# Performance work log

Hardware: AMD Instinct MI355X
Metric: run time of the kernel (lower is better)

The kernel has to match this reference:

```python
import jax, jax.numpy as jnp
import numpy as np

# torch.linspace(512, 16, 3).int() -> [512, 264, 16]
RES = (512, 264, 16)
FEAT = 4
EMBED_DIM = 1 + FEAT * len(RES)  # 13
HID = 64
N = 4194304


def _linear_init(key, fan_in, fan_out):
    k1, k2 = jax.random.split(key)
    bound = 1.0 / np.sqrt(fan_in)
    w = jax.random.uniform(k1, (fan_in, fan_out), jnp.float32, -bound, bound)
    b = jax.random.uniform(k2, (fan_out,), jnp.float32, -bound, bound)
    return w, b


def setup_inputs() -> dict:
    key = jax.random.key(0)
    ks = jax.random.split(key, 8)
    x = jax.random.uniform(ks[0], (N, 3), jnp.float32)  # [idf, u, v], uv in [0,1)
    tabs = []
    for i, r in enumerate(RES):
        tabs.append(jax.random.uniform(ks[1 + i], ((r + 1) * (r + 1), FEAT),
                                       jnp.float32, -1e-4, 1e-4))
    w1, b1 = _linear_init(ks[4], EMBED_DIM, HID)
    w2, b2 = _linear_init(ks[5], HID, HID)
    w3, b3 = _linear_init(ks[6], HID, 3)
    return {"x": x, "emb0": tabs[0], "emb1": tabs[1], "emb2": tabs[2],
            "w1": w1, "b1": b1, "w2": w2, "b2": b2, "w3": w3, "b3": b3}


def _grid_features(uv, tables):
    feats = []
    for tab, res in zip(tables, RES):
        sx = uv[:, 0] * res
        sy = uv[:, 1] * res
        x0 = sx.astype(jnp.int32)
        y0 = sy.astype(jnp.int32)
        wx = (sx - x0.astype(jnp.float32))[:, None]
        wy = (sy - y0.astype(jnp.float32))[:, None]
        x1 = jnp.minimum(x0 + 1, res)
        y1 = jnp.minimum(y0 + 1, res)
        # note: stride is res (not res+1), faithful to the original code
        v00 = tab[y0 * res + x0]
        v10 = tab[y0 * res + x1]
        v01 = tab[y1 * res + x0]
        v11 = tab[y1 * res + x1]
        top = v00 * (1.0 - wx) + v10 * wx
        bot = v01 * (1.0 - wx) + v11 * wx
        feats.append(top * (1.0 - wy) + bot * wy)
    return jnp.concatenate(feats, axis=1)


def reference(x, emb0, emb1, emb2, w1, b1, w2, b2, w3, b3):
    idf = x[:, :1]
    uv = x[:, 1:3]
    dgf = _grid_features(uv, (emb0, emb1, emb2))
    h = jnp.concatenate([idf, dgf], axis=1)  # [N, 13]
    h = jax.nn.relu(h @ w1 + b1)
    h = jax.nn.relu(h @ w2 + b2)
    return h @ w3 + b3  # [N, 3]
```

## Files before the change

### kernel.cpp

```cpp
#include <hip/hip_runtime.h>

typedef _Float16 half8 __attribute__((ext_vector_type(8)));
typedef _Float16 half4 __attribute__((ext_vector_type(4)));
typedef _Float16 h2    __attribute__((ext_vector_type(2)));
typedef __fp16  fp16x2 __attribute__((ext_vector_type(2)));
typedef float floatx4 __attribute__((ext_vector_type(4)));
typedef float floatx2 __attribute__((ext_vector_type(2)));
typedef int   intx4  __attribute__((ext_vector_type(4)));
typedef intx4 intx4a __attribute__((aligned(8)));

#define TPB 256
#define SCALE   8192.0f
#define INVSC   0.0001220703125f

#define N0E (512 * 512 + 1)
#define N1E (264 * 264 + 1)
#define NC2 (16 * 16)

struct GAddr { int i00, i10, i01, i11; float wx, wy; };

__device__ __forceinline__ GAddr gaddr(int res, float u, float v) {
    float r = (float)res;
    float sx = u * r, sy = v * r;
    int x0 = (int)sx, y0 = (int)sy;
    float wx = sx - (float)x0, wy = sy - (float)y0;
    int x1 = min(x0 + 1, res), y1 = min(y0 + 1, res);
    GAddr g;
    g.i00 = y0 * res + x0;  g.i10 = y0 * res + x1;
    g.i01 = y1 * res + x0;  g.i11 = y1 * res + x1;
    g.wx = wx; g.wy = wy;
    return g;
}

struct GQ { int c; float wx, wy; };

__device__ __forceinline__ GQ gq(int res, float u, float v) {
    float r = (float)res;
    float sx = u * r, sy = v * r;
    int x0 = (int)sx, y0 = (int)sy;
    GQ g; g.c = y0 * res + x0; g.wx = sx - (float)x0; g.wy = sy - (float)y0;
    return g;
}

__device__ __forceinline__ void bil4(float4 v00, float4 v10, float4 v01, float4 v11,
                                     float wx, float wy, float* f) {
    float omx = 1.0f - wx, omy = 1.0f - wy;
    f[0] = (v00.x * omx + v10.x * wx) * omy + (v01.x * omx + v11.x * wx) * wy;
    f[1] = (v00.y * omx + v10.y * wx) * omy + (v01.y * omx + v11.y * wx) * wy;
    f[2] = (v00.z * omx + v10.z * wx) * omy + (v01.z * omx + v11.z * wx) * wy;
    f[3] = (v00.w * omx + v10.w * wx) * omy + (v01.w * omx + v11.w * wx) * wy;
}

__device__ __forceinline__ h2 pk2(float a, float b) {
    fp16x2 r = __builtin_amdgcn_cvt_pkrtz(a, b);
    union { fp16x2 f; h2 h; } u; u.f = r; return u.h;
}

__device__ __forceinline__ void bil8(intx4 q, float wx, float omyS, float wyS, float* f) {
    floatx2 a00 = __builtin_amdgcn_cvt_pk_f32_fp8(q.x, false);
    floatx2 b00 = __builtin_amdgcn_cvt_pk_f32_fp8(q.x, true);
    floatx2 a01 = __builtin_amdgcn_cvt_pk_f32_fp8(q.y, false);
    floatx2 b01 = __builtin_amdgcn_cvt_pk_f32_fp8(q.y, true);
    floatx2 a10 = __builtin_amdgcn_cvt_pk_f32_fp8(q.z, false);
    floatx2 b10 = __builtin_amdgcn_cvt_pk_f32_fp8(q.z, true);
    floatx2 a11 = __builtin_amdgcn_cvt_pk_f32_fp8(q.w, false);
    floatx2 b11 = __builtin_amdgcn_cvt_pk_f32_fp8(q.w, true);
    float omx = 1.0f - wx;
    f[0] = (a00[0] * omx + a10[0] * wx) * omyS + (a01[0] * omx + a11[0] * wx) * wyS;
    f[1] = (a00[1] * omx + a10[1] * wx) * omyS + (a01[1] * omx + a11[1] * wx) * wyS;
    f[2] = (b00[0] * omx + b10[0] * wx) * omyS + (b01[0] * omx + b11[0] * wx) * wyS;
    f[3] = (b00[1] * omx + b10[1] * wx) * omyS + (b01[1] * omx + b11[1] * wx) * wyS;
}

__device__ __forceinline__ void bilq(half8 q0, half8 q1, float wx, float wy, h2* f) {
    h2 wx2  = pk2(wx, wx),           wy2  = pk2(wy, wy);
    h2 omx2 = pk2(1.f - wx, 1.f - wx), omy2 = pk2(1.f - wy, 1.f - wy);
    union { half8 v; h2 p[4]; } a, b;
    a.v = q0; b.v = q1;
    h2 t0 = a.p[0] * omx2 + a.p[2] * wx2;
    h2 t1 = a.p[1] * omx2 + a.p[3] * wx2;
    h2 c0 = b.p[0] * omx2 + b.p[2] * wx2;
    h2 c1 = b.p[1] * omx2 + b.p[3] * wx2;
    f[0] = t0 * omy2 + c0 * wy2;
    f[1] = t1 * omy2 + c1 * wy2;
}

__device__ __forceinline__ half4 relu_pk4(float a, float b, float c, float d) {
    union { half4 v; h2 p[2]; } u;
    u.p[0] = pk2(a, b);
    u.p[1] = pk2(c, d);
    half4 z = {(_Float16)0, (_Float16)0, (_Float16)0, (_Float16)0};
    return __builtin_elementwise_max(u.v, z);
}

__device__ __forceinline__ half4 relu_pk4f(float a, float b, float c, float d) {
    union { half4 v; fp16x2 p[2]; } u;
    u.p[0] = __builtin_amdgcn_cvt_pkrtz(fmaxf(a, 0.0f), fmaxf(b, 0.0f));
    u.p[1] = __builtin_amdgcn_cvt_pkrtz(fmaxf(c, 0.0f), fmaxf(d, 0.0f));
    return u.v;
}

__global__ void pack_tables(const float4* __restrict__ e0,
                            const float4* __restrict__ e1,
                            const float4* __restrict__ e2,
                            int* __restrict__ w)
{
    int i = blockIdx.x * blockDim.x + threadIdx.x;
    if (i < N0E) {
        float4 A = e0[i];
        float4 C = e0[i + 512];
        int d0 = __builtin_amdgcn_cvt_pk_fp8_f32(A.x * SCALE, A.y * SCALE, 0, false);
        d0     = __builtin_amdgcn_cvt_pk_fp8_f32(A.z * SCALE, A.w * SCALE, d0, true);
        int d1 = __builtin_amdgcn_cvt_pk_fp8_f32(C.x * SCALE, C.y * SCALE, 0, false);
        d1     = __builtin_amdgcn_cvt_pk_fp8_f32(C.z * SCALE, C.w * SCALE, d1, true);
        w[2 * i] = d0; w[2 * i + 1] = d1;
    } else if (i < N0E + N1E) {
        int c = i - N0E;
        float4 A = e1[c];
        float4 C = e1[c + 264];
        int d0 = __builtin_amdgcn_cvt_pk_fp8_f32(A.x * SCALE, A.y * SCALE, 0, false);
        d0     = __builtin_amdgcn_cvt_pk_fp8_f32(A.z * SCALE, A.w * SCALE, d0, true);
        int d1 = __builtin_amdgcn_cvt_pk_fp8_f32(C.x * SCALE, C.y * SCALE, 0, false);
        d1     = __builtin_amdgcn_cvt_pk_fp8_f32(C.z * SCALE, C.w * SCALE, d1, true);
        w[2 * (N0E + c)] = d0; w[2 * (N0E + c) + 1] = d1;
    } else if (i < N0E + N1E + NC2) {
        int c = i - N0E - N1E;
        float4 A = e2[c], B = e2[c + 1], C = e2[c + 16], D = e2[c + 17];
        half8* q = (half8*)(w + 2 * (N0E + N1E));
        union { half8 v; h2 p[4]; } u0, u1;
        u0.p[0] = pk2(A.x, A.y); u0.p[1] = pk2(A.z, A.w);
        u0.p[2] = pk2(B.x, B.y); u0.p[3] = pk2(B.z, B.w);
        u1.p[0] = pk2(C.x, C.y); u1.p[1] = pk2(C.z, C.w);
        u1.p[2] = pk2(D.x, D.y); u1.p[3] = pk2(D.z, D.w);
        q[2 * c]     = u0.v;
        q[2 * c + 1] = u1.v;
    }
}

__global__ __launch_bounds__(TPB, 3) void dgn_mfma(
    const float* __restrict__ x,
    const int2*  __restrict__ tabs,
    const float*  __restrict__ w1, const float* __restrict__ b1,
    const float*  __restrict__ w2, const float* __restrict__ b2,
    const float*  __restrict__ w3, const float* __restrict__ b3,
    float*        __restrict__ out, int npts)
{
    __shared__ __align__(16) _Float16 smem[4 * 4096];
    __shared__ __align__(16) _Float16 w2l[4096];
    __shared__ __align__(16) _Float16 e2l[4096];

    const int2*  p0  = tabs;
    const int2*  p1  = tabs + N0E;
    const half8* q2t = (const half8*)(tabs + N0E + N1E);

    const int tid  = threadIdx.x;
    const int lane = tid & 63;
    const int wv   = tid >> 6;
    const int l15  = lane & 15;
    const int quad = lane >> 4;

    for (int e = tid; e < 4096; e += TPB) {
        int nt = e >> 10, rem = e & 1023, lw = rem >> 6, s = rem & 63;
        int oh = ((s & 3) << 4) | (s >> 2);
        w2l[nt * 1024 + lw * 64 + (s ^ ((lw & 7) << 3))] =
            (_Float16)w2[oh * 64 + nt * 16 + lw];
    }
    for (int e = tid; e < 2 * NC2; e += TPB)
        ((half8*)e2l)[e] = q2t[e];
    __syncthreads();

    half8 w1f[4];
    #pragma unroll
    for (int nt = 0; nt < 4; ++nt)
        #pragma unroll
        for (int j = 0; j < 8; ++j) {
            int k = quad * 8 + j;
            int row = (k < 12) ? (k + 1) : ((k == 12) ? 0 : -1);
            w1f[nt][j] = (row >= 0) ? (_Float16)w1[row * 64 + nt * 16 + l15] : (_Float16)0.0f;
        }
    float b1v[4], b2v[4];
    #pragma unroll
    for (int nt = 0; nt < 4; ++nt) { b1v[nt] = b1[nt * 16 + l15]; b2v[nt] = b2[nt * 16 + l15]; }
    half8 w3f[2];
    #pragma unroll
    for (int ks = 0; ks < 2; ++ks)
        #pragma unroll
        for (int j = 0; j < 8; ++j) {
            int s  = ks * 32 + quad * 8 + j;
            int oh = ((s & 3) << 4) | (s >> 2);
            w3f[ks][j] = (l15 < 3) ? (_Float16)w3[oh * 3 + l15] : (_Float16)0.0f;
        }
    const float qsel = (quad == 0) ? 1.0f : 0.0f;
    const float qb30 = qsel * b3[0], qb31 = qsel * b3[1], qb32 = qsel * b3[2];

    const int bufh = wv * 4096;
    const int ewr0 = bufh + lane * 64 + ((lane & 7) ^ 0) * 8;
    const int ewr1 = bufh + lane * 64 + ((lane & 7) ^ 1) * 8;
    const int erd  = bufh + l15 * 64 + (quad ^ (l15 & 7)) * 8;
    int hwb[4];
    #pragma unroll
    for (int r = 0; r < 4; ++r) {
        int pr = quad * 4 + r;
        hwb[r] = bufh + pr * 64 + (((l15 >> 1) ^ (pr & 7)) * 8) + (l15 & 1) * 4;
    }
    int rd2[2];
    #pragma unroll
    for (int ks = 0; ks < 2; ++ks)
        rd2[ks] = bufh + l15 * 64 + (((ks * 4 + quad) ^ (l15 & 7)) * 8);
    int w2a[2];
    #pragma unroll
    for (int ks = 0; ks < 2; ++ks)
        w2a[ks] = l15 * 64 + (((ks * 4 + quad) ^ (l15 & 7)) * 8);

    const int ntiles = npts >> 8;
    const int gdim   = gridDim.x;

    float cidf, cu, cv;
    float nidf, nu, nv;
    float wx0, wy0, wx1, wy1;
    intx4 t0q, t1q;
    {
        int p0i = (blockIdx.x << 8) + (wv << 6) + lane;
        cidf = x[3 * p0i]; cu = x[3 * p0i + 1]; cv = x[3 * p0i + 2];
        int tn = blockIdx.x + gdim;
        int p1i = (((tn < ntiles) ? tn : blockIdx.x) << 8) + (wv << 6) + lane;
        nidf = x[3 * p1i]; nu = x[3 * p1i + 1]; nv = x[3 * p1i + 2];
        GQ g0 = gq(512, cu, cv); wx0 = g0.wx; wy0 = g0.wy;
        t0q = *(const intx4a*)&p0[g0.c];
        GQ g1 = gq(264, cu, cv); wx1 = g1.wx; wy1 = g1.wy;
        t1q = *(const intx4a*)&p1[g1.c];
    }

    for (int tile = blockIdx.x; tile < ntiles; tile += gdim) {
        float nwx0, nwy0, nwx1, nwy1;
        intx4 m0q, m1q;
        {
            GQ g0 = gq(512, nu, nv); nwx0 = g0.wx; nwy0 = g0.wy;
            m0q = *(const intx4a*)&p0[g0.c];
            GQ g1 = gq(264, nu, nv); nwx1 = g1.wx; nwy1 = g1.wy;
            m1q = *(const intx4a*)&p1[g1.c];
        }

        int nxt2 = tile + 2 * gdim;
        int ptn = (((nxt2 < ntiles) ? nxt2 : tile) << 8) + (wv << 6) + lane;
        float fidf = x[3 * ptn], fu = x[3 * ptn + 1], fv = x[3 * ptn + 2];

        float f0[4], f1[4];
        bil8(t0q, wx0, (1.0f - wy0) * INVSC, wy0 * INVSC, f0);
        bil8(t1q, wx1, (1.0f - wy1) * INVSC, wy1 * INVSC, f1);
        h2 F2[2];
        {
            GQ g2 = gq(16, cu, cv);
            half8 qa = *(const half8*)&e2l[g2.c * 16];
            half8 qb = *(const half8*)&e2l[g2.c * 16 + 8];
            bilq(qa, qb, g2.wx, g2.wy, F2);
        }
        union H8 { half8 v; h2 p[4]; } e0u, e1u;
        e0u.p[0] = pk2(f0[0], f0[1]); e0u.p[1] = pk2(f0[2], f0[3]);
        e0u.p[2] = pk2(f1[0], f1[1]); e0u.p[3] = pk2(f1[2], f1[3]);
        e1u.p[0] = F2[0]; e1u.p[1] = F2[1];
        e1u.p[2] = pk2(cidf, 0.0f); e1u.p[3] = pk2(0.0f, 0.0f);
        *(half8*)&smem[ewr0] = e0u.v;
        *(half8*)&smem[ewr1] = e1u.v;

        #pragma unroll
        for (int mt = 0; mt < 4; ++mt) {
            half8 ea = { (_Float16)0, (_Float16)0, (_Float16)0, (_Float16)0,
                         (_Float16)0, (_Float16)0, (_Float16)0, (_Float16)0 };
            if (quad < 2) ea = *(const half8*)&smem[erd + mt * 1024];
            floatx4 acc[4];
            #pragma unroll
            for (int nt = 0; nt < 4; ++nt) {
                acc[nt] = (floatx4){ b1v[nt], b1v[nt], b1v[nt], b1v[nt] };
                acc[nt] = __builtin_amdgcn_mfma_f32_16x16x32_f16(ea, w1f[nt], acc[nt], 0, 0, 0);
            }
            #pragma unroll
            for (int r = 0; r < 4; ++r)
                *(half4*)&smem[hwb[r] + mt * 1024] =
                    relu_pk4(acc[0][r], acc[1][r], acc[2][r], acc[3][r]);
        }

        half8 w2r[4][2];
        #pragma unroll
        for (int nt = 0; nt < 4; ++nt)
            #pragma unroll
            for (int ks = 0; ks < 2; ++ks)
                w2r[nt][ks] = *(const half8*)&w2l[nt * 1024 + w2a[ks]];
        #pragma unroll
        for (int mt = 0; mt < 4; ++mt) {
            floatx4 acc[4];
            #pragma unroll
            for (int nt = 0; nt < 4; ++nt)
                acc[nt] = (floatx4){ b2v[nt], b2v[nt], b2v[nt], b2v[nt] };
            #pragma unroll
            for (int ks = 0; ks < 2; ++ks) {
                half8 a2 = *(const half8*)&smem[rd2[ks] + mt * 1024];
                #pragma unroll
                for (int nt = 0; nt < 4; ++nt)
                    acc[nt] = __builtin_amdgcn_mfma_f32_16x16x32_f16(a2, w2r[nt][ks], acc[nt], 0, 0, 0);
            }
            #pragma unroll
            for (int r = 0; r < 4; ++r)
                *(half4*)&smem[hwb[r] + mt * 1024] =
                    relu_pk4(acc[0][r], acc[1][r], acc[2][r], acc[3][r]);
        }

        #pragma unroll
        for (int mt = 0; mt < 4; ++mt) {
            floatx4 acc3 = (floatx4){ qb30, qb31, qb32, 0.0f };
            #pragma unroll
            for (int ks = 0; ks < 2; ++ks) {
                half8 bfr = *(const half8*)&smem[rd2[ks] + mt * 1024];
                acc3 = __builtin_amdgcn_mfma_f32_16x16x32_f16(w3f[ks], bfr, acc3, 0, 0, 0);
            }
            if (quad == 0) {
                const int P = (tile << 8) + (wv << 6) + mt * 16 + l15;
                out[3 * P + 0] = acc3[0];
                out[3 * P + 1] = acc3[1];
                out[3 * P + 2] = acc3[2];
            }
        }

        cidf = nidf; cu = nu; cv = nv;
        nidf = fidf; nu = fu; nv = fv;
        wx0 = nwx0; wy0 = nwy0; wx1 = nwx1; wy1 = nwy1;
        t0q = m0q; t1q = m1q;
    }
}

__global__ __launch_bounds__(TPB, 3) void dgn_mfma_fb(
    const float*  __restrict__ x,
    const float4* __restrict__ emb0,
    const float4* __restrict__ emb1,
    const float4* __restrict__ emb2,
    const float*  __restrict__ w1, const float* __restrict__ b1,
    const float*  __restrict__ w2, const float* __restrict__ b2,
    const float*  __restrict__ w3, const float* __restrict__ b3,
    float*        __restrict__ out, int npts)
{
    __shared__ __align__(16) _Float16 smem[4 * 4096];
    __shared__ __align__(16) _Float16 w2l[4096];

    const int tid  = threadIdx.x;
    const int lane = tid & 63;
    const int wv   = tid >> 6;
    const int l15  = lane & 15;
    const int quad = lane >> 4;

    for (int e = tid; e < 4096; e += TPB) {
        int nt = e >> 10, rem = e & 1023, lw = rem >> 6, s = rem & 63;
        int oh = ((s & 3) << 4) | (s >> 2);
        w2l[nt * 1024 + lw * 64 + (s ^ ((lw & 7) << 3))] =
            (_Float16)w2[oh * 64 + nt * 16 + lw];
    }
    __syncthreads();

    half8 w1f[4];
    #pragma unroll
    for (int nt = 0; nt < 4; ++nt)
        #pragma unroll
        for (int j = 0; j < 8; ++j) {
            int k = quad * 8 + j;
            w1f[nt][j] = (k < 13) ? (_Float16)w1[k * 64 + nt * 16 + l15] : (_Float16)0.0f;
        }
    float b1v[4], b2v[4];
    #pragma unroll
    for (int nt = 0; nt < 4; ++nt) { b1v[nt] = b1[nt * 16 + l15]; b2v[nt] = b2[nt * 16 + l15]; }
    half8 w3f[2];
    #pragma unroll
    for (int ks = 0; ks < 2; ++ks)
        #pragma unroll
        for (int j = 0; j < 8; ++j) {
            int s  = ks * 32 + quad * 8 + j;
            int oh = ((s & 3) << 4) | (s >> 2);
            w3f[ks][j] = (l15 < 3) ? (_Float16)w3[oh * 3 + l15] : (_Float16)0.0f;
        }
    const float qsel = (quad == 0) ? 1.0f : 0.0f;
    const float qb30 = qsel * b3[0], qb31 = qsel * b3[1], qb32 = qsel * b3[2];

    const int bufh = wv * 4096;
    const int ewr0 = bufh + lane * 64 + ((lane & 7) ^ 0) * 8;
    const int ewr1 = bufh + lane * 64 + ((lane & 7) ^ 1) * 8;
    const int erd  = bufh + l15 * 64 + (quad ^ (l15 & 7)) * 8;
    int hwb[4];
    #pragma unroll
    for (int r = 0; r < 4; ++r) {
        int pr = quad * 4 + r;
        hwb[r] = bufh + pr * 64 + (((l15 >> 1) ^ (pr & 7)) * 8) + (l15 & 1) * 4;
    }
    int rd2[2];
    #pragma unroll
    for (int ks = 0; ks < 2; ++ks)
        rd2[ks] = bufh + l15 * 64 + (((ks * 4 + quad) ^ (l15 & 7)) * 8);
    int w2a[2];
    #pragma unroll
    for (int ks = 0; ks < 2; ++ks)
        w2a[ks] = l15 * 64 + (((ks * 4 + quad) ^ (l15 & 7)) * 8);

    const int ntiles = npts >> 8;
    const int gdim   = gridDim.x;

    float cidf, cu, cv, wx0, wy0, wx1, wy1;
    float4 t00, t01, t02, t03, t10, t11, t12, t13;
    {
        int p0 = (blockIdx.x << 8) + (wv << 6) + lane;
        cidf = x[3 * p0]; cu = x[3 * p0 + 1]; cv = x[3 * p0 + 2];
        GAddr g0 = gaddr(512, cu, cv); wx0 = g0.wx; wy0 = g0.wy;
        t00 = emb0[g0.i00]; t01 = emb0[g0.i10]; t02 = emb0[g0.i01]; t03 = emb0[g0.i11];
        GAddr g1 = gaddr(264, cu, cv); wx1 = g1.wx; wy1 = g1.wy;
        t10 = emb1[g1.i00]; t11 = emb1[g1.i10]; t12 = emb1[g1.i01]; t13 = emb1[g1.i11];
    }

    for (int tile = blockIdx.x; tile < ntiles; tile += gdim) {
        float f[12];
        bil4(t00, t01, t02, t03, wx0, wy0, f);
        bil4(t10, t11, t12, t13, wx1, wy1, f + 4);
        {
            GAddr g2 = gaddr(16, cu, cv);
            bil4(emb2[g2.i00], emb2[g2.i10], emb2[g2.i01], emb2[g2.i11], g2.wx, g2.wy, f + 8);
        }
        union H8 { half8 v; fp16x2 p[4]; } e0u, e1u;
        e0u.p[0] = __builtin_amdgcn_cvt_pkrtz(cidf, f[0]);
        e0u.p[1] = __builtin_amdgcn_cvt_pkrtz(f[1], f[2]);
        e0u.p[2] = __builtin_amdgcn_cvt_pkrtz(f[3], f[4]);
        e0u.p[3] = __builtin_amdgcn_cvt_pkrtz(f[5], f[6]);
        e1u.p[0] = __builtin_amdgcn_cvt_pkrtz(f[7], f[8]);
        e1u.p[1] = __builtin_amdgcn_cvt_pkrtz(f[9], f[10]);
        e1u.p[2] = __builtin_amdgcn_cvt_pkrtz(f[11], 0.0f);
        e1u.p[3] = __builtin_amdgcn_cvt_pkrtz(0.0f, 0.0f);
        *(half8*)&smem[ewr0] = e0u.v;
        *(half8*)&smem[ewr1] = e1u.v;

        int nxt = tile + gdim;
        int ptn = (((nxt < ntiles) ? nxt : tile) << 8) + (wv << 6) + lane;
        float nidf = x[3 * ptn], nu = x[3 * ptn + 1], nv = x[3 * ptn + 2];

        #pragma unroll
        for (int mt = 0; mt < 4; ++mt) {
            half8 ea = { (_Float16)0, (_Float16)0, (_Float16)0, (_Float16)0,
                         (_Float16)0, (_Float16)0, (_Float16)0, (_Float16)0 };
            if (quad < 2) ea = *(const half8*)&smem[erd + mt * 1024];
            floatx4 acc[4];
            #pragma unroll
            for (int nt = 0; nt < 4; ++nt) {
                acc[nt] = (floatx4){ b1v[nt], b1v[nt], b1v[nt], b1v[nt] };
                acc[nt] = __builtin_amdgcn_mfma_f32_16x16x32_f16(ea, w1f[nt], acc[nt], 0, 0, 0);
            }
            #pragma unroll
            for (int r = 0; r < 4; ++r)
                *(half4*)&smem[hwb[r] + mt * 1024] =
                    relu_pk4f(acc[0][r], acc[1][r], acc[2][r], acc[3][r]);
        }

        float nwx0, nwy0, nwx1, nwy1;
        float4 n00, n01, n02, n03, n10, n11, n12, n13;
        {
            GAddr g0 = gaddr(512, nu, nv); nwx0 = g0.wx; nwy0 = g0.wy;
            n00 = emb0[g0.i00]; n01 = emb0[g0.i10]; n02 = emb0[g0.i01]; n03 = emb0[g0.i11];
            GAddr g1 = gaddr(264, nu, nv); nwx1 = g1.wx; nwy1 = g1.wy;
            n10 = emb1[g1.i00]; n11 = emb1[g1.i10]; n12 = emb1[g1.i01]; n13 = emb1[g1.i11];
        }

        half8 w2r[4][2];
        #pragma unroll
        for (int nt = 0; nt < 4; ++nt)
            #pragma unroll
            for (int ks = 0; ks < 2; ++ks)
                w2r[nt][ks] = *(const half8*)&w2l[nt * 1024 + w2a[ks]];
        #pragma unroll
        for (int mt = 0; mt < 4; ++mt) {
            floatx4 acc[4];
            #pragma unroll
            for (int nt = 0; nt < 4; ++nt)
                acc[nt] = (floatx4){ b2v[nt], b2v[nt], b2v[nt], b2v[nt] };
            #pragma unroll
            for (int ks = 0; ks < 2; ++ks) {
                half8 a2 = *(const half8*)&smem[rd2[ks] + mt * 1024];
                #pragma unroll
                for (int nt = 0; nt < 4; ++nt)
                    acc[nt] = __builtin_amdgcn_mfma_f32_16x16x32_f16(a2, w2r[nt][ks], acc[nt], 0, 0, 0);
            }
            #pragma unroll
            for (int r = 0; r < 4; ++r)
                *(half4*)&smem[hwb[r] + mt * 1024] =
                    relu_pk4f(acc[0][r], acc[1][r], acc[2][r], acc[3][r]);
        }

        #pragma unroll
        for (int mt = 0; mt < 4; ++mt) {
            floatx4 acc3 = (floatx4){ qb30, qb31, qb32, 0.0f };
            #pragma unroll
            for (int ks = 0; ks < 2; ++ks) {
                half8 bfr = *(const half8*)&smem[rd2[ks] + mt * 1024];
                acc3 = __builtin_amdgcn_mfma_f32_16x16x32_f16(w3f[ks], bfr, acc3, 0, 0, 0);
            }
            if (quad == 0) {
                const int P = (tile << 8) + (wv << 6) + mt * 16 + l15;
                out[3 * P + 0] = acc3[0];
                out[3 * P + 1] = acc3[1];
                out[3 * P + 2] = acc3[2];
            }
        }

        cidf = nidf; cu = nu; cv = nv;
        wx0 = nwx0; wy0 = nwy0; wx1 = nwx1; wy1 = nwy1;
        t00 = n00; t01 = n01; t02 = n02; t03 = n03;
        t10 = n10; t11 = n11; t12 = n12; t13 = n13;
    }
}

extern "C" void kernel_launch(void* const* d_in, const int* in_sizes, int n_in,
                              void* d_out, int out_size, void* d_ws, size_t ws_size,
                              hipStream_t stream) {
    const float*  x    = (const float*)  d_in[0];
    const float4* emb0 = (const float4*) d_in[1];
    const float4* emb1 = (const float4*) d_in[2];
    const float4* emb2 = (const float4*) d_in[3];
    const float*  w1   = (const float*)  d_in[4];
    const float*  b1   = (const float*)  d_in[5];
    const float*  w2   = (const float*)  d_in[6];
    const float*  b2   = (const float*)  d_in[7];
    const float*  w3   = (const float*)  d_in[8];
    const float*  b3   = (const float*)  d_in[9];
    float* out = (float*)d_out;

    int npts = in_sizes[0] / 3;
    const size_t need = (size_t)(N0E + N1E) * 8 + (size_t)NC2 * 32;

    if (d_ws != nullptr && ws_size >= need) {
        int work = N0E + N1E + NC2;
        pack_tables<<<(work + 255) / 256, 256, 0, stream>>>(emb0, emb1, emb2, (int*)d_ws);
        dgn_mfma<<<768, TPB, 0, stream>>>(x, (const int2*)d_ws,
                                          w1, b1, w2, b2, w3, b3, out, npts);
    } else {
        dgn_mfma_fb<<<768, TPB, 0, stream>>>(x, emb0, emb1, emb2,
                                             w1, b1, w2, b2, w3, b3, out, npts);
    }
}
```

Measured before the change: 191.2 us.

## Unify level-2 grid into fp8 packed table, shorten prefetch depth, raise occupancy

```diff
diff --git a/kernel.cpp b/kernel.cpp
--- a/kernel.cpp
+++ b/kernel.cpp
@@ -15,7 +15,7 @@
 
 #define N0E (512 * 512 + 1)
 #define N1E (264 * 264 + 1)
-#define NC2 (16 * 16)
+#define N2E (16 * 16 + 2)
 
 struct GAddr { int i00, i10, i01, i11; float wx, wy; };
 
@@ -72,19 +72,6 @@
     f[3] = (b00[1] * omx + b10[1] * wx) * omyS + (b01[1] * omx + b11[1] * wx) * wyS;
 }
 
-__device__ __forceinline__ void bilq(half8 q0, half8 q1, float wx, float wy, h2* f) {
-    h2 wx2  = pk2(wx, wx),           wy2  = pk2(wy, wy);
-    h2 omx2 = pk2(1.f - wx, 1.f - wx), omy2 = pk2(1.f - wy, 1.f - wy);
-    union { half8 v; h2 p[4]; } a, b;
-    a.v = q0; b.v = q1;
-    h2 t0 = a.p[0] * omx2 + a.p[2] * wx2;
-    h2 t1 = a.p[1] * omx2 + a.p[3] * wx2;
-    h2 c0 = b.p[0] * omx2 + b.p[2] * wx2;
-    h2 c1 = b.p[1] * omx2 + b.p[3] * wx2;
-    f[0] = t0 * omy2 + c0 * wy2;
-    f[1] = t1 * omy2 + c1 * wy2;
-}
-
 __device__ __forceinline__ half4 relu_pk4(float a, float b, float c, float d) {
     union { half4 v; h2 p[2]; } u;
     u.p[0] = pk2(a, b);
@@ -106,38 +93,22 @@
                             int* __restrict__ w)
 {
     int i = blockIdx.x * blockDim.x + threadIdx.x;
-    if (i < N0E) {
-        float4 A = e0[i];
-        float4 C = e0[i + 512];
-        int d0 = __builtin_amdgcn_cvt_pk_fp8_f32(A.x * SCALE, A.y * SCALE, 0, false);
-        d0     = __builtin_amdgcn_cvt_pk_fp8_f32(A.z * SCALE, A.w * SCALE, d0, true);
-        int d1 = __builtin_amdgcn_cvt_pk_fp8_f32(C.x * SCALE, C.y * SCALE, 0, false);
-        d1     = __builtin_amdgcn_cvt_pk_fp8_f32(C.z * SCALE, C.w * SCALE, d1, true);
-        w[2 * i] = d0; w[2 * i + 1] = d1;
-    } else if (i < N0E + N1E) {
-        int c = i - N0E;
-        float4 A = e1[c];
-        float4 C = e1[c + 264];
-        int d0 = __builtin_amdgcn_cvt_pk_fp8_f32(A.x * SCALE, A.y * SCALE, 0, false);
-        d0     = __builtin_amdgcn_cvt_pk_fp8_f32(A.z * SCALE, A.w * SCALE, d0, true);
-        int d1 = __builtin_amdgcn_cvt_pk_fp8_f32(C.x * SCALE, C.y * SCALE, 0, false);
-        d1     = __builtin_amdgcn_cvt_pk_fp8_f32(C.z * SCALE, C.w * SCALE, d1, true);
-        w[2 * (N0E + c)] = d0; w[2 * (N0E + c) + 1] = d1;
-    } else if (i < N0E + N1E + NC2) {
-        int c = i - N0E - N1E;
-        float4 A = e2[c], B = e2[c + 1], C = e2[c + 16], D = e2[c + 17];
-        half8* q = (half8*)(w + 2 * (N0E + N1E));
-        union { half8 v; h2 p[4]; } u0, u1;
-        u0.p[0] = pk2(A.x, A.y); u0.p[1] = pk2(A.z, A.w);
-        u0.p[2] = pk2(B.x, B.y); u0.p[3] = pk2(B.z, B.w);
-        u1.p[0] = pk2(C.x, C.y); u1.p[1] = pk2(C.z, C.w);
-        u1.p[2] = pk2(D.x, D.y); u1.p[3] = pk2(D.z, D.w);
-        q[2 * c]     = u0.v;
-        q[2 * c + 1] = u1.v;
-    }
-}
-
-__global__ __launch_bounds__(TPB, 3) void dgn_mfma(
+    const float4* src; int res, base, c;
+    if (i < N0E)                       { src = e0; res = 512; base = 0;          c = i; }
+    else if (i < N0E + N1E)            { src = e1; res = 264; base = N0E;        c = i - N0E; }
+    else if (i < N0E + N1E + N2E)      { src = e2; res = 16;  base = N0E + N1E;  c = i - N0E - N1E; }
+    else return;
+    float4 A = src[c];
+    float4 C = src[c + res];
+    int d0 = __builtin_amdgcn_cvt_pk_fp8_f32(A.x * SCALE, A.y * SCALE, 0, false);
+    d0     = __builtin_amdgcn_cvt_pk_fp8_f32(A.z * SCALE, A.w * SCALE, d0, true);
+    int d1 = __builtin_amdgcn_cvt_pk_fp8_f32(C.x * SCALE, C.y * SCALE, 0, false);
+    d1     = __builtin_amdgcn_cvt_pk_fp8_f32(C.z * SCALE, C.w * SCALE, d1, true);
+    w[2 * (base + c)]     = d0;
+    w[2 * (base + c) + 1] = d1;
+}
+
+__global__ __launch_bounds__(TPB, 4) void dgn_mfma(
     const float* __restrict__ x,
     const int2*  __restrict__ tabs,
     const float*  __restrict__ w1, const float* __restrict__ b1,
@@ -147,11 +118,10 @@
 {
     __shared__ __align__(16) _Float16 smem[4 * 4096];
     __shared__ __align__(16) _Float16 w2l[4096];
-    __shared__ __align__(16) _Float16 e2l[4096];
-
-    const int2*  p0  = tabs;
-    const int2*  p1  = tabs + N0E;
-    const half8* q2t = (const half8*)(tabs + N0E + N1E);
+
+    const int2* p0 = tabs;
+    const int2* p1 = tabs + N0E;
+    const int2* p2 = tabs + N0E + N1E;
 
     const int tid  = threadIdx.x;
     const int lane = tid & 63;
@@ -165,8 +135,6 @@
         w2l[nt * 1024 + lw * 64 + (s ^ ((lw & 7) << 3))] =
             (_Float16)w2[oh * 64 + nt * 16 + lw];
     }
-    for (int e = tid; e < 2 * NC2; e += TPB)
-        ((half8*)e2l)[e] = q2t[e];
     __syncthreads();
 
     half8 w1f[4];
@@ -215,69 +183,62 @@
     const int ntiles = npts >> 8;
     const int gdim   = gridDim.x;
 
-    float cidf, cu, cv;
-    float nidf, nu, nv;
-    float wx0, wy0, wx1, wy1;
-    intx4 t0q, t1q;
+    float cidf, cu, cv, wx0, wy0, wx1, wy1, wx2, wy2;
+    intx4 t0q, t1q, t2q;
     {
-        int p0i = (blockIdx.x << 8) + (wv << 6) + lane;
-        cidf = x[3 * p0i]; cu = x[3 * p0i + 1]; cv = x[3 * p0i + 2];
-        int tn = blockIdx.x + gdim;
-        int p1i = (((tn < ntiles) ? tn : blockIdx.x) << 8) + (wv << 6) + lane;
-        nidf = x[3 * p1i]; nu = x[3 * p1i + 1]; nv = x[3 * p1i + 2];
+        int pi = (blockIdx.x << 8) + (wv << 6) + lane;
+        cidf = x[3 * pi]; cu = x[3 * pi + 1]; cv = x[3 * pi + 2];
         GQ g0 = gq(512, cu, cv); wx0 = g0.wx; wy0 = g0.wy;
         t0q = *(const intx4a*)&p0[g0.c];
         GQ g1 = gq(264, cu, cv); wx1 = g1.wx; wy1 = g1.wy;
         t1q = *(const intx4a*)&p1[g1.c];
+        GQ g2 = gq(16, cu, cv); wx2 = g2.wx; wy2 = g2.wy;
+        t2q = *(const intx4a*)&p2[g2.c];
     }
 
     for (int tile = blockIdx.x; tile < ntiles; tile += gdim) {
-        float nwx0, nwy0, nwx1, nwy1;
-        intx4 m0q, m1q;
+        float f0[4], f1[4], f2[4];
+        bil8(t0q, wx0, (1.0f - wy0) * INVSC, wy0 * INVSC, f0);
+        bil8(t1q, wx1, (1.0f - wy1) * INVSC, wy1 * INVSC, f1);
+        bil8(t2q, wx2, (1.0f - wy2) * INVSC, wy2 * INVSC, f2);
+        union H8 { half8 v; h2 p[4]; } e0u, e1u;
+        e0u.p[0] = pk2(f0[0], f0[1]); e0u.p[1] = pk2(f0[2], f0[3]);
+        e0u.p[2] = pk2(f1[0], f1[1]); e0u.p[3] = pk2(f1[2], f1[3]);
+        e1u.p[0] = pk2(f2[0], f2[1]); e1u.p[1] = pk2(f2[2], f2[3]);
+        e1u.p[2] = pk2(cidf, 0.0f);   e1u.p[3] = pk2(0.0f, 0.0f);
+        *(half8*)&smem[ewr0] = e0u.v;
+        *(half8*)&smem[ewr1] = e1u.v;
+
+        int nxt = tile + gdim;
+        int ptn = (((nxt < ntiles) ? nxt : tile) << 8) + (wv << 6) + lane;
+        float nidf = x[3 * ptn], nu = x[3 * ptn + 1], nv = x[3 * ptn + 2];
+
+        #pragma unroll
+        for (int mt = 0; mt < 4; ++mt) {
+            half8 ea = { (_Float16)0, (_Float16)0, (_Float16)0, (_Float16)0,
+                         (_Float16)0, (_Float16)0, (_Float16)0, (_Float16)0 };
+            if (quad < 2) ea = *(const half8*)&smem[erd + mt * 1024];
+            floatx4 acc[4];
+            #pragma unroll
+            for (int nt = 0; nt < 4; ++nt) {
+                acc[nt] = (floatx4){ b1v[nt], b1v[nt], b1v[nt], b1v[nt] };
+                acc[nt] = __builtin_amdgcn_mfma_f32_16x16x32_f16(ea, w1f[nt], acc[nt], 0, 0, 0);
+            }
+            #pragma unroll
+            for (int r = 0; r < 4; ++r)
+                *(half4*)&smem[hwb[r] + mt * 1024] =
+                    relu_pk4(acc[0][r], acc[1][r], acc[2][r], acc[3][r]);
+        }
+
+        float nwx0, nwy0, nwx1, nwy1, nwx2, nwy2;
+        intx4 m0q, m1q, m2q;
         {
             GQ g0 = gq(512, nu, nv); nwx0 = g0.wx; nwy0 = g0.wy;
             m0q = *(const intx4a*)&p0[g0.c];
             GQ g1 = gq(264, nu, nv); nwx1 = g1.wx; nwy1 = g1.wy;
             m1q = *(const intx4a*)&p1[g1.c];
-        }
-
-        int nxt2 = tile + 2 * gdim;
-        int ptn = (((nxt2 < ntiles) ? nxt2 : tile) << 8) + (wv << 6) + lane;
-        float fidf = x[3 * ptn], fu = x[3 * ptn + 1], fv = x[3 * ptn + 2];
-
-        float f0[4], f1[4];
-        bil8(t0q, wx0, (1.0f - wy0) * INVSC, wy0 * INVSC, f0);
-        bil8(t1q, wx1, (1.0f - wy1) * INVSC, wy1 * INVSC, f1);
-        h2 F2[2];
-        {
-            GQ g2 = gq(16, cu, cv);
-            half8 qa = *(const half8*)&e2l[g2.c * 16];
-            half8 qb = *(const half8*)&e2l[g2.c * 16 + 8];
-            bilq(qa, qb, g2.wx, g2.wy, F2);
-        }
-        union H8 { half8 v; h2 p[4]; } e0u, e1u;
-        e0u.p[0] = pk2(f0[0], f0[1]); e0u.p[1] = pk2(f0[2], f0[3]);
-        e0u.p[2] = pk2(f1[0], f1[1]); e0u.p[3] = pk2(f1[2], f1[3]);
-        e1u.p[0] = F2[0]; e1u.p[1] = F2[1];
-        e1u.p[2] = pk2(cidf, 0.0f); e1u.p[3] = pk2(0.0f, 0.0f);
-        *(half8*)&smem[ewr0] = e0u.v;
-        *(half8*)&smem[ewr1] = e1u.v;
-
-        #pragma unroll
-        for (int mt = 0; mt < 4; ++mt) {
-            half8 ea = { (_Float16)0, (_Float16)0, (_Float16)0, (_Float16)0,
-                         (_Float16)0, (_Float16)0, (_Float16)0, (_Float16)0 };
-            if (quad < 2) ea = *(const half8*)&smem[erd + mt * 1024];
-            floatx4 acc[4];
-            #pragma unroll
-            for (int nt = 0; nt < 4; ++nt) {
-                acc[nt] = (floatx4){ b1v[nt], b1v[nt], b1v[nt], b1v[nt] };
-                acc[nt] = __builtin_amdgcn_mfma_f32_16x16x32_f16(ea, w1f[nt], acc[nt], 0, 0, 0);
-            }
-            #pragma unroll
-            for (int r = 0; r < 4; ++r)
-                *(half4*)&smem[hwb[r] + mt * 1024] =
-                    relu_pk4(acc[0][r], acc[1][r], acc[2][r], acc[3][r]);
+            GQ g2 = gq(16, nu, nv); nwx2 = g2.wx; nwy2 = g2.wy;
+            m2q = *(const intx4a*)&p2[g2.c];
         }
 
         half8 w2r[4][2];
@@ -322,9 +283,8 @@
         }
 
         cidf = nidf; cu = nu; cv = nv;
-        nidf = fidf; nu = fu; nv = fv;
-        wx0 = nwx0; wy0 = nwy0; wx1 = nwx1; wy1 = nwy1;
-        t0q = m0q; t1q = m1q;
+        wx0 = nwx0; wy0 = nwy0; wx1 = nwx1; wy1 = nwy1; wx2 = nwx2; wy2 = nwy2;
+        t0q = m0q; t1q = m1q; t2q = m2q;
     }
 }
 
@@ -525,13 +485,13 @@
     float* out = (float*)d_out;
 
     int npts = in_sizes[0] / 3;
-    const size_t need = (size_t)(N0E + N1E) * 8 + (size_t)NC2 * 32;
+    const size_t need = (size_t)(N0E + N1E + N2E) * 8;
 
     if (d_ws != nullptr && ws_size >= need) {
-        int work = N0E + N1E + NC2;
+        int work = N0E + N1E + N2E;
         pack_tables<<<(work + 255) / 256, 256, 0, stream>>>(emb0, emb1, emb2, (int*)d_ws);
-        dgn_mfma<<<768, TPB, 0, stream>>>(x, (const int2*)d_ws,
-                                          w1, b1, w2, b2, w3, b3, out, npts);
+        dgn_mfma<<<1024, TPB, 0, stream>>>(x, (const int2*)d_ws,
+                                           w1, b1, w2, b2, w3, b3, out, npts);
     } else {
         dgn_mfma_fb<<<768, TPB, 0, stream>>>(x, emb0, emb1, emb2,
                                              w1, b1, w2, b2, w3, b3, out, npts);
```

Result: slower. 233.0 us (+21.9%).
